# Kernel optimization log

Hardware: AMD Instinct MI355X
Metric: run time of the kernel (lower is better)

## Reference

```python
import jax, jax.numpy as jnp
import numpy as np

H = 1.0  # primo_h
N_GRID = 768


def _grid_mesh(n):
    ii, jj = np.meshgrid(np.arange(n - 1), np.arange(n - 1), indexing='ij')
    v00 = (ii * n + jj).ravel(); v10 = ((ii + 1) * n + jj).ravel()
    v01 = (ii * n + jj + 1).ravel(); v11 = ((ii + 1) * n + jj + 1).ravel()
    tri1 = np.stack([v00, v10, v01], 1); tri2 = np.stack([v10, v11, v01], 1)
    return np.concatenate([tri1, tri2], 0).astype(np.int32)  # [F,3]


def _face_adjacency(faces):
    # faces: [F,3] -> edges [E,2] (sorted vertex pairs), face_ids [E,2]
    F = faces.shape[0]
    fe = np.stack([faces[:, [0, 1]], faces[:, [1, 2]], faces[:, [2, 0]]], 1).reshape(-1, 2)
    fe = np.sort(fe, axis=1)
    fid = np.repeat(np.arange(F, dtype=np.int32), 3)
    order = np.lexsort((fe[:, 1], fe[:, 0]))
    fs, fi = fe[order], fid[order]
    same = np.all(fs[:-1] == fs[1:], axis=1)
    k = np.nonzero(same)[0]
    edges = fs[k].astype(np.int32)
    face_ids = np.stack([fi[k], fi[k + 1]], 1).astype(np.int32)
    return edges, face_ids


def setup_inputs() -> dict:
    key = jax.random.key(0)
    k1, k2, k3 = jax.random.split(key, 3)
    faces_np = _grid_mesh(N_GRID)                      # [F,3]
    edges_np, face_ids_np = _face_adjacency(faces_np)  # [E,2],[E,2]
    F = faces_np.shape[0]
    V = N_GRID * N_GRID
    return {
        'transformed_prism': jax.random.normal(k1, (F, 3, 3), dtype=jnp.float32),
        'rotations': jax.random.normal(k2, (F, 3, 3), dtype=jnp.float32),
        'verts': jax.random.normal(k3, (1, V, 3), dtype=jnp.float32),
        'faces': jnp.asarray(faces_np.T),       # [3,F], matches torch forward arg
        'edges': jnp.asarray(edges_np),
        'face_ids': jnp.asarray(face_ids_np),
    }


def _verts_id_face(Ft, E, Q):
    # Ft: [F,3] faces; E: [e,2] edge vertex ids; Q: [e,2] adjacent face ids
    fa, fb = Ft[Q[:, 0]], Ft[Q[:, 1]]  # [e,3]

    def find(fv, tgt):
        return jnp.where(fv[:, 0] == tgt, 0,
               jnp.where(fv[:, 1] == tgt, 1,
               jnp.where(fv[:, 2] == tgt, 2, -1)))

    return jnp.stack([find(fa, E[:, 0]), find(fa, E[:, 1]),
                      find(fb, E[:, 0]), find(fb, E[:, 1])], axis=1)  # [e,4]


def reference(transformed_prism, rotations, verts, faces, edges, face_ids):
    tp = transformed_prism
    bs = verts.shape[0]
    v = verts.reshape(-1, 3)
    Ft = faces.T  # [F,3]

    # per-face normals (vectorized version of the original per-face loop)
    e1 = tp[:, 0] - tp[:, 1]
    e2 = tp[:, 0] - tp[:, 2]
    nrm = jnp.cross(e1, e2)
    normals = nrm / jnp.linalg.norm(nrm, axis=-1, keepdims=True)  # [F,3]

    # face areas
    p1, p2, p3 = v[Ft[:, 0]], v[Ft[:, 1]], v[Ft[:, 2]]
    face_areas = 0.5 * jnp.linalg.norm(jnp.cross(p2 - p1, p3 - p1), axis=1)

    # faithful to original: normals indexed by edge VERTEX ids
    n1, n2 = normals[edges[:, 0]], normals[edges[:, 1]]
    fid1, fid2 = face_ids[:, 0], face_ids[:, 1]
    r1, r2 = rotations[fid1], rotations[fid2]

    ftv = _verts_id_face(Ft, edges, face_ids)  # [e,4]
    v1_p1, v2_p1 = tp[fid1, ftv[:, 0]], tp[fid1, ftv[:, 1]]
    v1_p2, v2_p2 = tp[fid2, ftv[:, 2]], tp[fid2, ftv[:, 3]]

    p1n1 = jnp.einsum('ec,ecd->ed', n1, r1)
    p1n2 = jnp.einsum('ec,ecd->ed', n2, r1)
    p2n1 = jnp.einsum('ec,ecd->ed', n1, r2)
    p2n2 = jnp.einsum('ec,ecd->ed', n2, r2)

    A = jnp.stack([v1_p1 + p1n1 * H, v2_p1 + p1n2 * H,
                   v1_p1 - p1n1 * H, v2_p1 - p1n2 * H], axis=1)  # [e,4,3]
    B = jnp.stack([v1_p2 + p2n1 * H, v2_p2 + p2n2 * H,
                   v1_p2 - p2n1 * H, v2_p2 - p2n2 * H], axis=1)
    D = A - B

    # coeff[p,q] = 2^{-|i_p-i_q|-|j_p-j_q|}, (i,j) over {0,1}^2
    idx = jnp.array([[0, 0], [0, 1], [1, 0], [1, 1]], dtype=jnp.float32)
    coeff = 2.0 ** (-jnp.abs(idx[:, None] - idx[None, :]).sum(-1))  # [4,4]
    pair = jnp.einsum('epc,eqc->epq', D, D)
    energy = (pair * coeff).sum((1, 2)) / 9.0  # [e]

    weight = jnp.sum((v[edges[:, 0]] - v[edges[:, 1]]) ** 2, axis=1) \
             / (face_areas[fid1] + face_areas[fid2])
    return (energy * weight).sum() / bs
```

## Files before the change

kernel.cpp:

```cpp
#include <hip/hip_runtime.h>


#define BI 4
#define BJ 64
#define FR (BI + 1)
#define FC (BJ + 1)
#define NR (BI + 1)
#define NC (BJ + 1)
#define VR (BI + 2)
#define VC (BJ + 2)

struct __attribute__((aligned(4))) F4s { float a, b, c, d; };
struct F3 { float x, y, z; };
struct R9 { float v[9]; };

__device__ __forceinline__ R9 load9(const float* __restrict__ p) {
    R9 r;
    F4s u0 = *(const F4s*)p;
    F4s u1 = *(const F4s*)(p + 4);
    r.v[0] = u0.a; r.v[1] = u0.b; r.v[2] = u0.c; r.v[3] = u0.d;
    r.v[4] = u1.a; r.v[5] = u1.b; r.v[6] = u1.c; r.v[7] = u1.d;
    r.v[8] = p[8];
    return r;
}

__device__ __forceinline__ int iclamp(int x, int lo, int hi) {
    return x < lo ? lo : (x > hi ? hi : x);
}

__device__ __forceinline__ F3 normal_of(const R9& r) {
    float e1x = r.v[0] - r.v[3], e1y = r.v[1] - r.v[4], e1z = r.v[2] - r.v[5];
    float e2x = r.v[0] - r.v[6], e2y = r.v[1] - r.v[7], e2z = r.v[2] - r.v[8];
    float nx = e1y * e2z - e1z * e2y;
    float ny = e1z * e2x - e1x * e2z;
    float nz = e1x * e2y - e1y * e2x;
    float inv = 1.0f / sqrtf(nx * nx + ny * ny + nz * nz);
    F3 o; o.x = nx * inv; o.y = ny * inv; o.z = nz * inv; return o;
}

__device__ __forceinline__ float tri_area_p(const float* p, const float* q,
                                            const float* r) {
    float ax = q[0] - p[0], ay = q[1] - p[1], az = q[2] - p[2];
    float bx = r[0] - p[0], by = r[1] - p[1], bz = r[2] - p[2];
    float cx = ay * bz - az * by, cy = az * bx - ax * bz, cz = ax * by - ay * bx;
    return 0.5f * sqrtf(cx * cx + cy * cy + cz * cz);
}

__device__ __forceinline__ float edge_ew(const float* u1, const float* u2,
                                         const float* w1, const float* w2,
                                         const float* rA, const float* rB,
                                         const F3& n1, const F3& n2,
                                         const float* pa, const float* pb,
                                         float asum) {
    float ux = u1[0] - u2[0], uy = u1[1] - u2[1], uz = u1[2] - u2[2];
    float wx = w1[0] - w2[0], wy = w1[1] - w2[1], wz = w1[2] - w2[2];

    float d0 = rA[0] - rB[0], d1 = rA[1] - rB[1], d2 = rA[2] - rB[2];
    float d3 = rA[3] - rB[3], d4 = rA[4] - rB[4], d5 = rA[5] - rB[5];
    float d6 = rA[6] - rB[6], d7 = rA[7] - rB[7], d8 = rA[8] - rB[8];

    float ax = n1.x * d0 + n1.y * d3 + n1.z * d6;
    float ay = n1.x * d1 + n1.y * d4 + n1.z * d7;
    float az = n1.x * d2 + n1.y * d5 + n1.z * d8;
    float bx = n2.x * d0 + n2.y * d3 + n2.z * d6;
    float by = n2.x * d1 + n2.y * d4 + n2.z * d7;
    float bz = n2.x * d2 + n2.y * d5 + n2.z * d8;

    float uu = ux * ux + uy * uy + uz * uz;
    float ww = wx * wx + wy * wy + wz * wz;
    float uw = ux * wx + uy * wy + uz * wz;
    float aa = ax * ax + ay * ay + az * az;
    float bb = bx * bx + by * by + bz * bz;
    float ab = ax * bx + ay * by + az * bz;
    float energy = (3.0f * (uu + ww + uw) + (aa + bb + ab)) * (1.0f / 9.0f);

    float dx = pa[0] - pb[0], dy = pa[1] - pb[1], dz = pa[2] - pb[2];
    return energy * (dx * dx + dy * dy + dz * dz) / asum;
}

__global__ __launch_bounds__(256) void fused_kernel(
        const float* __restrict__ tp,
        const float* __restrict__ rot,
        const float* __restrict__ verts,
        double* __restrict__ partials,
        int n) {
    const int m = n - 1;
    const int Q = m * m;
    const int tid = threadIdx.x;
    const int i0 = blockIdx.y * BI;
    const int j0 = blockIdx.x * BJ;
    const int w = tid >> 6;
    const int l = tid & 63;
    const int i = i0 + w;
    const int j = j0 + l;

    __shared__ float sT2[FR * FC * 9];
    __shared__ float sR2[FR * FC * 9];
    __shared__ float sN[NR * NC * 3];
    __shared__ float sV[VR * VC * 3];
    __shared__ double sred[4];

    int f1 = iclamp(i, 0, m - 1) * m + iclamp(j, 0, m - 1);
    R9 t1 = load9(tp  + (size_t)9 * f1);
    R9 r1 = load9(rot + (size_t)9 * f1);

    for (int idx = tid; idx < FR * FC; idx += 256) {
        int r = idx / FC, c = idx - r * FC;
        int gi = iclamp(i0 - 1 + r, 0, m - 1);
        int gj = iclamp(j0 - 1 + c, 0, m - 1);
        size_t f = (size_t)Q + (size_t)gi * m + gj;
        R9 a = load9(tp  + 9 * f);
        R9 b = load9(rot + 9 * f);
#pragma unroll
        for (int k = 0; k < 9; ++k) sT2[9 * idx + k] = a.v[k];
#pragma unroll
        for (int k = 0; k < 9; ++k) sR2[9 * idx + k] = b.v[k];
    }
    for (int idx = tid; idx < NR * NC; idx += 256) {
        int r = idx / NC, c = idx - r * NC;
        int gi = iclamp(i0 + r, 0, n - 1);
        int gj = iclamp(j0 + c, 0, n - 1);
        R9 a = load9(tp + 9 * ((size_t)gi * n + gj));
        F3 nm = normal_of(a);
        sN[3 * idx] = nm.x; sN[3 * idx + 1] = nm.y; sN[3 * idx + 2] = nm.z;
    }
    for (int idx = tid; idx < VR * VC; idx += 256) {
        int r = idx / VC, c = idx - r * VC;
        int gi = iclamp(i0 - 1 + r, 0, n - 1);
        int gj = iclamp(j0 - 1 + c, 0, n - 1);
        const float* p = verts + 3 * ((size_t)gi * n + gj);
        sV[3 * idx] = p[0]; sV[3 * idx + 1] = p[1]; sV[3 * idx + 2] = p[2];
    }

    __syncthreads();

    double term = 0.0;
    if (i < m && j < m) {
        const float* t2c = sT2 + 9 * ((w + 1) * FC + (l + 1));
        const float* r2c = sR2 + 9 * ((w + 1) * FC + (l + 1));
        const float* th  = sT2 + 9 * (w * FC + (l + 1));
        const float* rh  = sR2 + 9 * (w * FC + (l + 1));
        const float* tv  = sT2 + 9 * ((w + 1) * FC + l);
        const float* rv  = sR2 + 9 * ((w + 1) * FC + l);

        F3 nA = { sN[3 * (w * NC + l)],
                  sN[3 * (w * NC + l) + 1],
                  sN[3 * (w * NC + l) + 2] };
        F3 nB = { sN[3 * (w * NC + l + 1)],
                  sN[3 * (w * NC + l + 1) + 1],
                  sN[3 * (w * NC + l + 1) + 2] };
        F3 nC = { sN[3 * ((w + 1) * NC + l)],
                  sN[3 * ((w + 1) * NC + l) + 1],
                  sN[3 * ((w + 1) * NC + l) + 2] };

        const float* p00 = sV + 3 * ((w + 1) * VC + (l + 1));
        const float* p01 = sV + 3 * ((w + 1) * VC + (l + 2));
        const float* p10 = sV + 3 * ((w + 2) * VC + (l + 1));
        const float* p11 = sV + 3 * ((w + 2) * VC + (l + 2));
        const float* pup = sV + 3 * (w * VC + (l + 2));
        const float* plf = sV + 3 * ((w + 2) * VC + l);

        float a1   = tri_area_p(p00, p10, p01);
        float a2c  = tri_area_p(p10, p11, p01);
        float a2up = tri_area_p(p00, p01, pup);
        float a2lf = tri_area_p(plf, p10, p00);

        float sum = edge_ew(t1.v + 6, t2c + 6, t1.v + 3, t2c + 0, r1.v, r2c,
                            nB, nC, p01, p10, a1 + a2c);
        float eh = edge_ew(t1.v + 0, th + 0, t1.v + 6, th + 3, r1.v, rh,
                           nA, nB, p00, p01, a1 + a2up);
        float ev = edge_ew(t1.v + 0, tv + 6, t1.v + 3, tv + 3, r1.v, rv,
                           nA, nC, p00, p10, a1 + a2lf);
        sum += (i > 0 ? eh : 0.0f);
        sum += (j > 0 ? ev : 0.0f);
        term = (double)sum;
    }

#pragma unroll
    for (int off = 32; off > 0; off >>= 1) term += __shfl_down(term, off, 64);
    if (l == 0) sred[w] = term;
    __syncthreads();
    if (tid == 0)
        partials[blockIdx.y * gridDim.x + blockIdx.x] =
            sred[0] + sred[1] + sred[2] + sred[3];
}

__global__ __launch_bounds__(256) void finalize_kernel(
        const double* __restrict__ partials, int P, float* __restrict__ out) {
    double s = 0.0;
    for (int i = threadIdx.x; i < P; i += 256) s += partials[i];
#pragma unroll
    for (int off = 32; off > 0; off >>= 1) s += __shfl_down(s, off, 64);
    __shared__ double sred[4];
    int lane = threadIdx.x & 63, wid = threadIdx.x >> 6;
    if (lane == 0) sred[wid] = s;
    __syncthreads();
    if (threadIdx.x == 0) out[0] = (float)(sred[0] + sred[1] + sred[2] + sred[3]);
}

extern "C" void kernel_launch(void* const* d_in, const int* in_sizes, int n_in,
                              void* d_out, int out_size, void* d_ws, size_t ws_size,
                              hipStream_t stream) {
    const float* tp    = (const float*)d_in[0];
    const float* rot   = (const float*)d_in[1];
    const float* verts = (const float*)d_in[2];

    int V = in_sizes[2] / 3;
    int n = (int)(sqrtf((float)V) + 0.5f);
    int m = n - 1;

    double* partials = (double*)d_ws;
    float*  out      = (float*)d_out;

    dim3 grid((m + BJ - 1) / BJ, (m + BI - 1) / BI);
    int P = grid.x * grid.y;
    fused_kernel<<<grid, 256, 0, stream>>>(tp, rot, verts, partials, n);
    finalize_kernel<<<1, 256, 0, stream>>>(partials, P, out);
}
```

Measured before the change: 152.9 us.

## Stage shared-memory tiles with coalesced float4 row copies and batched loads

Replaces the per-element 9-float gather into shared memory with contiguous float4 copies of whole tile rows of tp, rot and verts. The left halo column is stored separately at the end of each row. All global loads are issued into registers before any shared-memory stores, so more loads are in flight at once. This cuts scattered, uncoalesced loads and index arithmetic. In exchange it needs more registers and hard-coded layout constants that assume BJ=64, and the edge clamping is delicate.

After: 148.8 us. -2.7%, faster.

```diff
diff --git a/kernel.cpp b/kernel.cpp
--- a/kernel.cpp
+++ b/kernel.cpp
@@ -3,12 +3,15 @@
 
 #define BI 4
 #define BJ 64
-#define FR (BI + 1)
-#define FC (BJ + 1)
-#define NR (BI + 1)
-#define NC (BJ + 1)
-#define VR (BI + 2)
-#define VC (BJ + 2)
+#define T2STRIDE 588
+#define VSTRIDE  200
+#define NSTRIDE  195
+#define T2_CH    720
+#define V_CH     294
+#define MAIN_CH  (2 * T2_CH + V_CH)
+#define MAIN_ITERS 7
+#define HALO_CNT 108
+#define NORM_CNT 325
 
 struct __attribute__((aligned(4))) F4s { float a, b, c, d; };
 struct F3 { float x, y, z; };
@@ -24,9 +27,8 @@
     return r;
 }
 
-__device__ __forceinline__ int iclamp(int x, int lo, int hi) {
-    return x < lo ? lo : (x > hi ? hi : x);
-}
+__device__ __forceinline__ int imin(int a, int b) { return a < b ? a : b; }
+__device__ __forceinline__ int imax(int a, int b) { return a > b ? a : b; }
 
 __device__ __forceinline__ F3 normal_of(const R9& r) {
     float e1x = r.v[0] - r.v[3], e1y = r.v[1] - r.v[4], e1z = r.v[2] - r.v[5];
@@ -86,6 +88,8 @@
         int n) {
     const int m = n - 1;
     const int Q = m * m;
+    const int F = 2 * Q;
+    const int V = n * n;
     const int tid = threadIdx.x;
     const int i0 = blockIdx.y * BI;
     const int j0 = blockIdx.x * BJ;
@@ -94,71 +98,121 @@
     const int i = i0 + w;
     const int j = j0 + l;
 
-    __shared__ float sT2[FR * FC * 9];
-    __shared__ float sR2[FR * FC * 9];
-    __shared__ float sN[NR * NC * 3];
-    __shared__ float sV[VR * VC * 3];
+    __shared__ __attribute__((aligned(16))) float sT2[5 * T2STRIDE];
+    __shared__ __attribute__((aligned(16))) float sR2[5 * T2STRIDE];
+    __shared__ __attribute__((aligned(16))) float sV[6 * VSTRIDE];
+    __shared__ float sN[5 * NSTRIDE];
     __shared__ double sred[4];
 
-    int f1 = iclamp(i, 0, m - 1) * m + iclamp(j, 0, m - 1);
+    int f1 = imin(i, m - 1) * m + imin(j, m - 1);
     R9 t1 = load9(tp  + (size_t)9 * f1);
     R9 r1 = load9(rot + (size_t)9 * f1);
 
-    for (int idx = tid; idx < FR * FC; idx += 256) {
-        int r = idx / FC, c = idx - r * FC;
-        int gi = iclamp(i0 - 1 + r, 0, m - 1);
-        int gj = iclamp(j0 - 1 + c, 0, m - 1);
-        size_t f = (size_t)Q + (size_t)gi * m + gj;
-        R9 a = load9(tp  + 9 * f);
-        R9 b = load9(rot + 9 * f);
-#pragma unroll
-        for (int k = 0; k < 9; ++k) sT2[9 * idx + k] = a.v[k];
-#pragma unroll
-        for (int k = 0; k < 9; ++k) sR2[9 * idx + k] = b.v[k];
-    }
-    for (int idx = tid; idx < NR * NC; idx += 256) {
-        int r = idx / NC, c = idx - r * NC;
-        int gi = iclamp(i0 + r, 0, n - 1);
-        int gj = iclamp(j0 + c, 0, n - 1);
-        R9 a = load9(tp + 9 * ((size_t)gi * n + gj));
-        F3 nm = normal_of(a);
-        sN[3 * idx] = nm.x; sN[3 * idx + 1] = nm.y; sN[3 * idx + 2] = nm.z;
-    }
-    for (int idx = tid; idx < VR * VC; idx += 256) {
-        int r = idx / VC, c = idx - r * VC;
-        int gi = iclamp(i0 - 1 + r, 0, n - 1);
-        int gj = iclamp(j0 - 1 + c, 0, n - 1);
-        const float* p = verts + 3 * ((size_t)gi * n + gj);
-        sV[3 * idx] = p[0]; sV[3 * idx + 1] = p[1]; sV[3 * idx + 2] = p[2];
+    float4 mval[MAIN_ITERS];
+    float* mdst[MAIN_ITERS];
+#pragma unroll
+    for (int it = 0; it < MAIN_ITERS; ++it) {
+        int s = tid + 256 * it;
+        bool act = s < MAIN_CH;
+        int sc = act ? s : 0;
+        const float* gp;
+        float* lp;
+        if (sc < 2 * T2_CH) {
+            int a = sc >= T2_CH;
+            int t = a ? sc - T2_CH : sc;
+            int r = t / 144, c = t - r * 144;
+            int gi = imin(i0 - 1 + r, m - 1);
+            int g = 9 * (Q + gi * m + j0) + 4 * c;
+            g = imin(g, 9 * F - 4);
+            gp = (a ? rot : tp) + g;
+            lp = (a ? sR2 : sT2) + r * T2STRIDE + 4 * c;
+        } else {
+            int t = sc - 2 * T2_CH;
+            int r = t / 49, c = t - r * 49;
+            int vr = imax(imin(i0 - 1 + r, n - 1), 0);
+            int g = 3 * (vr * n + j0) + 4 * c;
+            g = imin(g, 3 * V - 4);
+            gp = verts + g;
+            lp = sV + r * VSTRIDE + 4 * c;
+        }
+        F4s u = *(const F4s*)gp;
+        mval[it] = make_float4(u.a, u.b, u.c, u.d);
+        mdst[it] = act ? lp : nullptr;
+    }
+
+    float hval = 0.0f;
+    float* hdst = nullptr;
+    if (tid < HALO_CNT) {
+        if (tid < 90) {
+            int a = tid >= 45;
+            int t = a ? tid - 45 : tid;
+            int r = t / 9, k = t - 9 * r;
+            int gi = imin(i0 - 1 + r, m - 1);
+            int face = Q + gi * m + (j0 - 1);
+            hval = (a ? rot : tp)[9 * face + k];
+            hdst = (a ? sR2 : sT2) + r * T2STRIDE + 576 + k;
+        } else {
+            int t = tid - 90;
+            int r = t / 3, k = t - 3 * r;
+            int vr = imax(imin(i0 - 1 + r, n - 1), 0);
+            int g = imax(3 * (vr * n + (j0 - 1)) + k, 0);
+            hval = verts[g];
+            hdst = sV + r * VSTRIDE + 196 + k;
+        }
+    }
+
+    R9 nraw[2];
+    int nofs[2];
+#pragma unroll
+    for (int it = 0; it < 2; ++it) {
+        int s = tid + 256 * it;
+        bool act = s < NORM_CNT;
+        int sc = act ? s : 0;
+        int r = sc / 65, c = sc - 65 * r;
+        int gi = imin(i0 + r, n - 1);
+        int gj = imin(j0 + c, n - 1);
+        nraw[it] = load9(tp + (size_t)9 * (gi * n + gj));
+        nofs[it] = act ? (r * NSTRIDE + 3 * c) : -1;
+    }
+
+#pragma unroll
+    for (int it = 0; it < MAIN_ITERS; ++it)
+        if (mdst[it]) *(float4*)mdst[it] = mval[it];
+    if (hdst) *hdst = hval;
+#pragma unroll
+    for (int it = 0; it < 2; ++it) {
+        if (nofs[it] >= 0) {
+            F3 nm = normal_of(nraw[it]);
+            sN[nofs[it]] = nm.x; sN[nofs[it] + 1] = nm.y; sN[nofs[it] + 2] = nm.z;
+        }
     }
 
     __syncthreads();
 
     double term = 0.0;
     if (i < m && j < m) {
-        const float* t2c = sT2 + 9 * ((w + 1) * FC + (l + 1));
-        const float* r2c = sR2 + 9 * ((w + 1) * FC + (l + 1));
-        const float* th  = sT2 + 9 * (w * FC + (l + 1));
-        const float* rh  = sR2 + 9 * (w * FC + (l + 1));
-        const float* tv  = sT2 + 9 * ((w + 1) * FC + l);
-        const float* rv  = sR2 + 9 * ((w + 1) * FC + l);
-
-        F3 nA = { sN[3 * (w * NC + l)],
-                  sN[3 * (w * NC + l) + 1],
-                  sN[3 * (w * NC + l) + 2] };
-        F3 nB = { sN[3 * (w * NC + l + 1)],
-                  sN[3 * (w * NC + l + 1) + 1],
-                  sN[3 * (w * NC + l + 1) + 2] };
-        F3 nC = { sN[3 * ((w + 1) * NC + l)],
-                  sN[3 * ((w + 1) * NC + l) + 1],
-                  sN[3 * ((w + 1) * NC + l) + 2] };
-
-        const float* p00 = sV + 3 * ((w + 1) * VC + (l + 1));
-        const float* p01 = sV + 3 * ((w + 1) * VC + (l + 2));
-        const float* p10 = sV + 3 * ((w + 2) * VC + (l + 1));
-        const float* p11 = sV + 3 * ((w + 2) * VC + (l + 2));
-        const float* pup = sV + 3 * (w * VC + (l + 2));
-        const float* plf = sV + 3 * ((w + 2) * VC + l);
+        const float* t2c = sT2 + (w + 1) * T2STRIDE + 9 * l;
+        const float* r2c = sR2 + (w + 1) * T2STRIDE + 9 * l;
+        const float* th  = sT2 + w * T2STRIDE + 9 * l;
+        const float* rh  = sR2 + w * T2STRIDE + 9 * l;
+        int cm1 = l ? 9 * (l - 1) : 576;
+        const float* tv  = sT2 + (w + 1) * T2STRIDE + cm1;
+        const float* rv  = sR2 + (w + 1) * T2STRIDE + cm1;
+
+        const float* p00 = sV + (w + 1) * VSTRIDE + 3 * l;
+        const float* p01 = p00 + 3;
+        const float* p10 = sV + (w + 2) * VSTRIDE + 3 * l;
+        const float* p11 = p10 + 3;
+        const float* pup = sV + w * VSTRIDE + 3 * (l + 1);
+        int vm1 = l ? 3 * (l - 1) : 196;
+        const float* plf = sV + (w + 2) * VSTRIDE + vm1;
+
+        const float* na = sN + w * NSTRIDE + 3 * l;
+        const float* nb = na + 3;
+        const float* nc = sN + (w + 1) * NSTRIDE + 3 * l;
+        F3 nA = { na[0], na[1], na[2] };
+        F3 nB = { nb[0], nb[1], nb[2] };
+        F3 nC = { nc[0], nc[1], nc[2] };
 
         float a1   = tri_area_p(p00, p10, p01);
         float a2c  = tri_area_p(p10, p11, p01);
```
